# Optimization experiments

Measured on AMD Instinct MI355X. Metric: run time of the kernel, lower is better.

Reference implementation:

```python
import jax, jax.numpy as jnp
import numpy as np

DIM = 512
HEADS = 8
DIM_HEAD = 64
INNER = HEADS * DIM_HEAD  # 512
B, N = 4, 2048
EPS = 1e-5
DIFF = 1.0


def setup_inputs() -> dict:
    key = jax.random.key(0)
    ks = jax.random.split(key, 8)
    s = 1.0 / np.sqrt(DIM)
    return {
        "x": jax.random.normal(ks[0], (B, N, DIM), dtype=jnp.float32),
        "ln_w": jnp.ones((DIM,), jnp.float32),
        "ln_b": jnp.zeros((DIM,), jnp.float32),
        "wq": jax.random.uniform(ks[1], (INNER, DIM), jnp.float32, -s, s),
        "wk": jax.random.uniform(ks[2], (INNER, DIM), jnp.float32, -s, s),
        "wv_v": jax.random.uniform(ks[3], (INNER, DIM), jnp.float32, -s, s),  # weight-norm direction
        "wv_g": jax.random.uniform(ks[4], (INNER,), jnp.float32, 0.5, 1.5),   # weight-norm magnitude g
        "w_out": jax.random.uniform(ks[5], (DIM, INNER), jnp.float32, -s, s),
    }


def reference(x, ln_w, ln_b, wq, wk, wv_v, wv_g, w_out):
    # LayerNorm over last dim
    mu = jnp.mean(x, axis=-1, keepdims=True)
    var = jnp.mean(jnp.square(x - mu), axis=-1, keepdims=True)
    xn = (x - mu) * jax.lax.rsqrt(var + EPS) * ln_w + ln_b

    # weight-norm for V projection: W = g * v / ||v||_row (norm over dim=1)
    wv = wv_g[:, None] * wv_v / jnp.linalg.norm(wv_v, axis=1, keepdims=True)

    def proj(w):  # [b n (h d)] -> [b h n d]
        t = jnp.einsum('bnc,ec->bne', xn, w)
        return t.reshape(x.shape[0], x.shape[1], HEADS, DIM_HEAD).transpose(0, 2, 1, 3)

    q, k, v = proj(wq), proj(wk), proj(wv)

    scale = DIM_HEAD ** -0.5
    dots = jnp.einsum('bhid,bhjd->bhij', q, k) * scale
    attn = jax.nn.softmax(dots, axis=-1)
    out = jnp.einsum('bhij,bhjd->bhid', DIFF * attn, v)  # diff-scaled AV
    out = out.transpose(0, 2, 1, 3).reshape(x.shape[0], x.shape[1], INNER)
    return jnp.einsum('bne,ce->bnc', out, w_out)
```

## Files before the change

### kernel.cpp

```cpp
#include <hip/hip_runtime.h>
#include <hip/hip_bf16.h>
#include <stdint.h>

typedef __attribute__((ext_vector_type(8))) __bf16 bf16x8;
typedef __attribute__((ext_vector_type(8))) short short8;
typedef __attribute__((ext_vector_type(4))) float f32x4;

#define C1_QSCALE 0.18033688011112042f

__device__ __forceinline__ unsigned short f2bf(float f) {
    union { float f; unsigned int u; } v; v.f = f;
    unsigned int r = v.u + 0x7fffu + ((v.u >> 16) & 1u);
    return (unsigned short)(r >> 16);
}

__device__ __forceinline__ unsigned int cvtpk(float lo, float hi) {
    unsigned int r;
    asm("v_cvt_pk_bf16_f32 %0, %1, %2" : "=v"(r) : "v"(lo), "v"(hi));
    return r;
}

__device__ __forceinline__ float fexp2(float x) {
    float r;
    asm("v_exp_f32 %0, %1" : "=v"(r) : "v"(x));
    return r;
}

__device__ __forceinline__ void gl_lds16(const void* g, void* l) {
    __builtin_amdgcn_global_load_lds(
        (const __attribute__((address_space(1))) unsigned int*)g,
        (__attribute__((address_space(3))) unsigned int*)l, 16, 0, 0);
}

__device__ __forceinline__ f32x4 mfma16(bf16x8 a, bf16x8 b, f32x4 c) {
    return __builtin_amdgcn_mfma_f32_16x16x32_bf16(a, b, c, 0, 0, 0);
}

__global__ __launch_bounds__(256) void pre_kernel(
    const float* __restrict__ x, const float* __restrict__ lw,
    const float* __restrict__ lb, unsigned short* __restrict__ xn,
    const float* __restrict__ wq, const float* __restrict__ wk,
    const float* __restrict__ wv_v, const float* __restrict__ wv_g,
    const float* __restrict__ w_out,
    unsigned short* __restrict__ wqkv, unsigned short* __restrict__ woutb)
{
    const int t = threadIdx.x;
    if (blockIdx.x < 2048) {
        const int wv = t >> 6, l = t & 63;
        const int row = blockIdx.x * 4 + wv;
        const float* xr = x + (size_t)row * 512;
        const float4 a = *(const float4*)(xr + l*8);
        const float4 b = *(const float4*)(xr + l*8 + 4);
        float s  = (a.x + a.y) + (a.z + a.w) + (b.x + b.y) + (b.z + b.w);
        float sq = (a.x*a.x + a.y*a.y) + (a.z*a.z + a.w*a.w)
                 + (b.x*b.x + b.y*b.y) + (b.z*b.z + b.w*b.w);
        #pragma unroll
        for (int m = 1; m < 64; m <<= 1) { s += __shfl_xor(s, m); sq += __shfl_xor(sq, m); }
        const float mean = s * (1.f/512.f);
        const float var  = sq * (1.f/512.f) - mean*mean;
        const float rs   = rsqrtf(var + 1e-5f);
        const float4 w0 = *(const float4*)(lw + l*8);
        const float4 w1 = *(const float4*)(lw + l*8 + 4);
        const float4 c0 = *(const float4*)(lb + l*8);
        const float4 c1 = *(const float4*)(lb + l*8 + 4);
        uint4 o;
        o.x = cvtpk((a.x-mean)*rs*w0.x + c0.x, (a.y-mean)*rs*w0.y + c0.y);
        o.y = cvtpk((a.z-mean)*rs*w0.z + c0.z, (a.w-mean)*rs*w0.w + c0.w);
        o.z = cvtpk((b.x-mean)*rs*w1.x + c1.x, (b.y-mean)*rs*w1.y + c1.y);
        o.w = cvtpk((b.z-mean)*rs*w1.z + c1.z, (b.w-mean)*rs*w1.w + c1.w);
        *(uint4*)(xn + (size_t)row*512 + l*8) = o;
    } else {
        __shared__ float red[4];
        const int row = blockIdx.x - 2048;
        if (row < 1536) {
            const float* src;
            float scale = 1.0f;
            if (row < 512) src = wq + (size_t)row*512;
            else if (row < 1024) src = wk + (size_t)(row-512)*512;
            else {
                src = wv_v + (size_t)(row-1024)*512;
                float2 v = *(const float2*)(src + t*2);
                float sq = v.x*v.x + v.y*v.y;
                #pragma unroll
                for (int m = 1; m < 64; m <<= 1) sq += __shfl_xor(sq, m);
                if ((t & 63) == 0) red[t >> 6] = sq;
                __syncthreads();
                scale = wv_g[row-1024] * rsqrtf(red[0]+red[1]+red[2]+red[3]);
            }
            float2 v = *(const float2*)(src + t*2);
            ushort2 o; o.x = f2bf(v.x*scale); o.y = f2bf(v.y*scale);
            *(ushort2*)(wqkv + (size_t)row*512 + t*2) = o;
        } else {
            const int r = row - 1536;
            float2 v = *(const float2*)(w_out + (size_t)r*512 + t*2);
            ushort2 o; o.x = f2bf(v.x); o.y = f2bf(v.y);
            *(ushort2*)(woutb + (size_t)r*512 + t*2) = o;
        }
    }
}

template<int MODE, int BM, int BN>
__global__ __launch_bounds__(256) void gemm_nt(
    const unsigned short* __restrict__ A,
    const unsigned short* __restrict__ B,
    unsigned short* __restrict__ qo,
    unsigned short* __restrict__ ko,
    unsigned short* __restrict__ vo,
    float* __restrict__ outf)
{
    constexpr int MT  = BM / 32;
    constexpr int NT  = BN / 32;
    constexpr int ACH = BM / 64;
    constexpr int BCH = BN / 64;
    constexpr int BUFSZ = (BM + BN) * 64;
    __shared__ __align__(16) unsigned char L[3][BUFSZ];

    const int t = threadIdx.x;
    const int wv = t >> 6, l = t & 63;
    const int brow = blockIdx.x * BM;
    const int bcol = blockIdx.y * BN;
    const int wr = (wv >> 1) * (BM/2), wc = (wv & 1) * (BN/2);
    const int l15 = l & 15, l4 = l >> 4;
    const int rl  = l >> 2;
    const int cbl = l & 3;

    const f32x4 fz = {0.f, 0.f, 0.f, 0.f};
    f32x4 acc[MT][NT];
    #pragma unroll
    for (int i = 0; i < MT; ++i)
        #pragma unroll
        for (int j = 0; j < NT; ++j) acc[i][j] = fz;

    auto STAGE = [&](int ks, int buf) {
        #pragma unroll
        for (int i = 0; i < ACH; ++i) {
            const int c = wv*ACH + i;
            const int row = c*16 + rl;
            const int scb = cbl ^ ((row >> 1) & 3);
            gl_lds16(A + (size_t)(brow+row)*512 + ks*32 + scb*8, &L[buf][c*1024]);
        }
        #pragma unroll
        for (int i = 0; i < BCH; ++i) {
            const int c = wv*BCH + i;
            const int row = c*16 + rl;
            const int scb = cbl ^ ((row >> 1) & 3);
            gl_lds16(B + (size_t)(bcol+row)*512 + ks*32 + scb*8, &L[buf][BM*64 + c*1024]);
        }
    };

    STAGE(0, 0);
    STAGE(1, 1);

    int cur = 0;
    for (int ks = 0; ks < 16; ++ks) {
        if constexpr (ACH + BCH == 4) asm volatile("s_waitcnt vmcnt(4)" ::: "memory");
        else                          asm volatile("s_waitcnt vmcnt(3)" ::: "memory");
        __builtin_amdgcn_s_barrier();

        int nb = cur + 2; if (nb >= 3) nb -= 3;
        STAGE((ks + 2) & 15, nb);

        bf16x8 af[MT], bfr[NT];
        #pragma unroll
        for (int mt = 0; mt < MT; ++mt) {
            const int row = wr + mt*16 + l15;
            af[mt] = *(const bf16x8*)(&L[cur][0] + row*64 + ((l4 ^ ((row >> 1) & 3))*16));
        }
        #pragma unroll
        for (int nt = 0; nt < NT; ++nt) {
            const int row = wc + nt*16 + l15;
            bfr[nt] = *(const bf16x8*)(&L[cur][BM*64] + row*64 + ((l4 ^ ((row >> 1) & 3))*16));
        }
        __builtin_amdgcn_s_setprio(1);
        #pragma unroll
        for (int mt = 0; mt < MT; ++mt)
            #pragma unroll
            for (int nt = 0; nt < NT; ++nt)
                acc[mt][nt] = mfma16(af[mt], bfr[nt], acc[mt][nt]);
        __builtin_amdgcn_s_setprio(0);

        cur = (cur == 2) ? 0 : cur + 1;
    }

    if (MODE == 1) {
        #pragma unroll
        for (int mt = 0; mt < MT; ++mt)
            #pragma unroll
            for (int nt = 0; nt < NT; ++nt)
                #pragma unroll
                for (int r = 0; r < 4; ++r) {
                    const int grow = brow + wr + mt*16 + l4*4 + r;
                    const int gcol = bcol + wc + nt*16 + l15;
                    outf[(size_t)grow*512 + gcol] = acc[mt][nt][r];
                }
    } else if (bcol < 1024) {
        const bool isq = (bcol < 512);
        unsigned short* dst = isq ? qo : ko;
        const int csub = isq ? bcol : bcol - 512;
        const float scl = isq ? C1_QSCALE : 1.0f;
        #pragma unroll
        for (int mt = 0; mt < MT; ++mt)
            #pragma unroll
            for (int nt = 0; nt < NT; ++nt)
                #pragma unroll
                for (int r = 0; r < 4; ++r) {
                    const int grow = brow + wr + mt*16 + l4*4 + r;
                    const int gcol = csub + wc + nt*16 + l15;
                    const int h = gcol >> 6, d = gcol & 63;
                    const int bb = grow >> 11, n = grow & 2047;
                    dst[(((size_t)bb*8 + h)*2048 + n)*64 + d] = f2bf(acc[mt][nt][r]*scl);
                }
    } else {
        #pragma unroll
        for (int mt = 0; mt < MT; ++mt) {
            const int grow0 = brow + wr + mt*16 + l4*4;
            const int bb = grow0 >> 11;
            const int nb2 = (grow0 & 2047) & ~63;
            const int sigma0 = (mt>>1)*32 + l4*8 + (mt&1)*4;
            #pragma unroll
            for (int nt = 0; nt < NT; ++nt) {
                const int gcol = (bcol - 1024) + wc + nt*16 + l15;
                const int h = gcol >> 6, d = gcol & 63;
                uint2 ov;
                ov.x = cvtpk(acc[mt][nt][0], acc[mt][nt][1]);
                ov.y = cvtpk(acc[mt][nt][2], acc[mt][nt][3]);
                *(uint2*)(vo + ((size_t)(bb*8 + h)*64 + d)*2048 + nb2 + sigma0) = ov;
            }
        }
    }
}

__global__ __launch_bounds__(512, 4) void flash_attn(
    const unsigned short* __restrict__ Q,
    const unsigned short* __restrict__ K,
    const unsigned short* __restrict__ Vt,
    unsigned short* __restrict__ AO)
{
    __shared__ __align__(16) unsigned char Ks[3][8192];
    __shared__ __align__(16) unsigned char Vs[2][8192];
    const int t = threadIdx.x, wv = t >> 6, l = t & 63;
    const int l15 = l & 15, l4 = l >> 4;
    const int rl = l >> 3, cbl = l & 7;
    const int bh = blockIdx.x;
    const int q0 = blockIdx.y * 128;
    const size_t base = (size_t)bh * 2048 * 64;
    const int b = bh >> 3, h = bh & 7;

    bf16x8 qf[2];
    #pragma unroll
    for (int kk = 0; kk < 2; ++kk)
        qf[kk] = *(const bf16x8*)(Q + base + (size_t)(q0 + wv*16 + l15)*64 + kk*32 + 8*l4);

    const f32x4 fz = {0.f,0.f,0.f,0.f};
    f32x4 acco[4];
    float lrp = 0.f;
    #pragma unroll
    for (int dn = 0; dn < 4; ++dn) acco[dn] = fz;

    auto STAGE_K = [&](int kv, int buf) {
        const int row = wv*8 + rl;
        const int scb = cbl ^ (row & 7);
        gl_lds16(K + base + (size_t)(kv + row)*64 + scb*8, &Ks[buf][wv*1024]);
    };
    auto STAGE_V = [&](int kv, int buf) {
        const int row = wv*8 + rl;
        const int scb = cbl ^ (row & 7);
        gl_lds16(Vt + base + (size_t)row*2048 + kv + scb*8, &Vs[buf][wv*1024]);
    };

    STAGE_V(0, 0);
    STAGE_K(0, 0);
    STAGE_K(64, 1);

    int kb = 0, vb = 0;
    for (int it = 0; it < 32; ++it) {
        asm volatile("s_waitcnt vmcnt(1)" ::: "memory");
        __builtin_amdgcn_s_barrier();

        STAGE_V(((it + 1) & 31) * 64, vb ^ 1);
        STAGE_K(((it + 2) & 31) * 64, kb >= 1 ? kb - 1 : 2);

        bf16x8 kf[4][2];
        #pragma unroll
        for (int nt = 0; nt < 4; ++nt)
            #pragma unroll
            for (int kk = 0; kk < 2; ++kk) {
                const int row = nt*16 + l15;
                const int cb = kk*4 + l4;
                kf[nt][kk] = *(const bf16x8*)(&Ks[kb][0] + row*128 + ((cb ^ (row & 7))*16));
            }
        f32x4 st[4];
        __builtin_amdgcn_s_setprio(1);
        #pragma unroll
        for (int nt = 0; nt < 4; ++nt) {
            st[nt] = mfma16(kf[nt][0], qf[0], fz);
            st[nt] = mfma16(kf[nt][1], qf[1], st[nt]);
        }
        __builtin_amdgcn_s_setprio(0);

        float p[4][4];
        #pragma unroll
        for (int nt = 0; nt < 4; ++nt)
            #pragma unroll
            for (int r = 0; r < 4; ++r) p[nt][r] = fexp2(st[nt][r]);
        float s0 = (p[0][0]+p[0][1]) + (p[0][2]+p[0][3]);
        float s1 = (p[1][0]+p[1][1]) + (p[1][2]+p[1][3]);
        float s2 = (p[2][0]+p[2][1]) + (p[2][2]+p[2][3]);
        float s3 = (p[3][0]+p[3][1]) + (p[3][2]+p[3][3]);
        lrp += (s0 + s1) + (s2 + s3);

        bf16x8 pb[2];
        #pragma unroll
        for (int kh = 0; kh < 2; ++kh) {
            union { unsigned int u[4]; bf16x8 v; } pu;
            pu.u[0] = cvtpk(p[2*kh][0],   p[2*kh][1]);
            pu.u[1] = cvtpk(p[2*kh][2],   p[2*kh][3]);
            pu.u[2] = cvtpk(p[2*kh+1][0], p[2*kh+1][1]);
            pu.u[3] = cvtpk(p[2*kh+1][2], p[2*kh+1][3]);
            pb[kh] = pu.v;
        }

        __builtin_amdgcn_s_setprio(1);
        #pragma unroll
        for (int dn = 0; dn < 4; ++dn)
            #pragma unroll
            for (int kh = 0; kh < 2; ++kh) {
                const int row = dn*16 + l15;
                const int cb = kh*4 + l4;
                const bf16x8 vf = *(const bf16x8*)(&Vs[vb][0] + row*128 + ((cb ^ (row & 7))*16));
                acco[dn] = mfma16(vf, pb[kh], acco[dn]);
            }
        __builtin_amdgcn_s_setprio(0);

        kb = (kb == 2) ? 0 : kb + 1;
        vb ^= 1;
    }

    float lr = lrp;
    lr += __shfl_xor(lr, 16);
    lr += __shfl_xor(lr, 32);
    const float inv = 1.f / lr;
    const size_t nrow = (size_t)b*2048 + q0 + wv*16 + l15;
    #pragma unroll
    for (int dn = 0; dn < 4; ++dn) {
        uint2 ov;
        ov.x = cvtpk(acco[dn][0]*inv, acco[dn][1]*inv);
        ov.y = cvtpk(acco[dn][2]*inv, acco[dn][3]*inv);
        *(uint2*)(AO + nrow*512 + h*64 + dn*16 + l4*4) = ov;
    }
}

extern "C" void kernel_launch(void* const* d_in, const int* in_sizes, int n_in,
                              void* d_out, int out_size, void* d_ws, size_t ws_size,
                              hipStream_t stream)
{
    const float* x     = (const float*)d_in[0];
    const float* ln_w  = (const float*)d_in[1];
    const float* ln_b  = (const float*)d_in[2];
    const float* wq    = (const float*)d_in[3];
    const float* wk    = (const float*)d_in[4];
    const float* wv_v  = (const float*)d_in[5];
    const float* wv_g  = (const float*)d_in[6];
    const float* w_out = (const float*)d_in[7];
    float* out = (float*)d_out;
    char* ws = (char*)d_ws;

    unsigned short* xn    = (unsigned short*)(ws);
    unsigned short* ao    = (unsigned short*)(ws);
    unsigned short* wqkv  = (unsigned short*)(ws +  8388608);
    unsigned short* woutb = (unsigned short*)(ws +  9961472);
    unsigned short* q     = (unsigned short*)(ws + 10485760);
    unsigned short* k     = (unsigned short*)(ws + 18874368);
    unsigned short* vt    = (unsigned short*)(ws + 27262976);

    pre_kernel<<<dim3(4096), dim3(256), 0, stream>>>(x, ln_w, ln_b, xn,
        wq, wk, wv_v, wv_g, w_out, wqkv, woutb);
    gemm_nt<0,128,128><<<dim3(64, 12), dim3(256), 0, stream>>>(xn, wqkv, q, k, vt, (float*)nullptr);
    flash_attn<<<dim3(32, 16), dim3(512), 0, stream>>>(q, k, vt, ao);
    gemm_nt<1,128,64><<<dim3(64, 8), dim3(256), 0, stream>>>(ao, woutb,
        (unsigned short*)nullptr, (unsigned short*)nullptr, (unsigned short*)nullptr, out);
}
```

Baseline: 148.4 us.

## Process two query sub-tiles per wave to reuse K/V fragments in flash attention

Each wave now handles 32 query rows (two 16-row sub-tiles) instead of 16, so every K and V fragment read from LDS feeds two MFMAs. The block covers 256 queries, the grid along queries is halved, and launch bounds drop to 2 blocks per CU to allow more registers. The goal is to halve LDS traffic and global K/V staging per query. The cost is higher register pressure, fewer resident waves for hiding latency, and a smaller grid (256 blocks) that may leave some CUs idle.

```diff
diff --git a/kernel.cpp b/kernel.cpp
--- a/kernel.cpp
+++ b/kernel.cpp
@@ -230,7 +230,7 @@
     }
 }
 
-__global__ __launch_bounds__(512, 4) void flash_attn(
+__global__ __launch_bounds__(512, 2) void flash_attn(
     const unsigned short* __restrict__ Q,
     const unsigned short* __restrict__ K,
     const unsigned short* __restrict__ Vt,
@@ -242,20 +242,24 @@
     const int l15 = l & 15, l4 = l >> 4;
     const int rl = l >> 3, cbl = l & 7;
     const int bh = blockIdx.x;
-    const int q0 = blockIdx.y * 128;
+    const int q0 = blockIdx.y * 256;
     const size_t base = (size_t)bh * 2048 * 64;
     const int b = bh >> 3, h = bh & 7;
 
-    bf16x8 qf[2];
+    bf16x8 qf[2][2];
     #pragma unroll
-    for (int kk = 0; kk < 2; ++kk)
-        qf[kk] = *(const bf16x8*)(Q + base + (size_t)(q0 + wv*16 + l15)*64 + kk*32 + 8*l4);
+    for (int hq = 0; hq < 2; ++hq)
+        #pragma unroll
+        for (int kk = 0; kk < 2; ++kk)
+            qf[hq][kk] = *(const bf16x8*)(Q + base + (size_t)(q0 + wv*32 + hq*16 + l15)*64 + kk*32 + 8*l4);
 
     const f32x4 fz = {0.f,0.f,0.f,0.f};
-    f32x4 acco[4];
-    float lrp = 0.f;
+    f32x4 acco[2][4];
+    float lrp[2] = {0.f, 0.f};
     #pragma unroll
-    for (int dn = 0; dn < 4; ++dn) acco[dn] = fz;
+    for (int hq = 0; hq < 2; ++hq)
+        #pragma unroll
+        for (int dn = 0; dn < 4; ++dn) acco[hq][dn] = fz;
 
     auto STAGE_K = [&](int kv, int buf) {
         const int row = wv*8 + rl;
@@ -289,35 +293,39 @@
                 const int cb = kk*4 + l4;
                 kf[nt][kk] = *(const bf16x8*)(&Ks[kb][0] + row*128 + ((cb ^ (row & 7))*16));
             }
-        f32x4 st[4];
-        __builtin_amdgcn_s_setprio(1);
-        #pragma unroll
-        for (int nt = 0; nt < 4; ++nt) {
-            st[nt] = mfma16(kf[nt][0], qf[0], fz);
-            st[nt] = mfma16(kf[nt][1], qf[1], st[nt]);
-        }
-        __builtin_amdgcn_s_setprio(0);
-
-        float p[4][4];
-        #pragma unroll
-        for (int nt = 0; nt < 4; ++nt)
-            #pragma unroll
-            for (int r = 0; r < 4; ++r) p[nt][r] = fexp2(st[nt][r]);
-        float s0 = (p[0][0]+p[0][1]) + (p[0][2]+p[0][3]);
-        float s1 = (p[1][0]+p[1][1]) + (p[1][2]+p[1][3]);
-        float s2 = (p[2][0]+p[2][1]) + (p[2][2]+p[2][3]);
-        float s3 = (p[3][0]+p[3][1]) + (p[3][2]+p[3][3]);
-        lrp += (s0 + s1) + (s2 + s3);
-
-        bf16x8 pb[2];
-        #pragma unroll
-        for (int kh = 0; kh < 2; ++kh) {
-            union { unsigned int u[4]; bf16x8 v; } pu;
-            pu.u[0] = cvtpk(p[2*kh][0],   p[2*kh][1]);
-            pu.u[1] = cvtpk(p[2*kh][2],   p[2*kh][3]);
-            pu.u[2] = cvtpk(p[2*kh+1][0], p[2*kh+1][1]);
-            pu.u[3] = cvtpk(p[2*kh+1][2], p[2*kh+1][3]);
-            pb[kh] = pu.v;
+
+        bf16x8 pb[2][2];
+        #pragma unroll
+        for (int hq = 0; hq < 2; ++hq) {
+            f32x4 st[4];
+            __builtin_amdgcn_s_setprio(1);
+            #pragma unroll
+            for (int nt = 0; nt < 4; ++nt) {
+                st[nt] = mfma16(kf[nt][0], qf[hq][0], fz);
+                st[nt] = mfma16(kf[nt][1], qf[hq][1], st[nt]);
+            }
+            __builtin_amdgcn_s_setprio(0);
+
+            float p[4][4];
+            #pragma unroll
+            for (int nt = 0; nt < 4; ++nt)
+                #pragma unroll
+                for (int r = 0; r < 4; ++r) p[nt][r] = fexp2(st[nt][r]);
+            float s0 = (p[0][0]+p[0][1]) + (p[0][2]+p[0][3]);
+            float s1 = (p[1][0]+p[1][1]) + (p[1][2]+p[1][3]);
+            float s2 = (p[2][0]+p[2][1]) + (p[2][2]+p[2][3]);
+            float s3 = (p[3][0]+p[3][1]) + (p[3][2]+p[3][3]);
+            lrp[hq] += (s0 + s1) + (s2 + s3);
+
+            #pragma unroll
+            for (int kh = 0; kh < 2; ++kh) {
+                union { unsigned int u[4]; bf16x8 v; } pu;
+                pu.u[0] = cvtpk(p[2*kh][0],   p[2*kh][1]);
+                pu.u[1] = cvtpk(p[2*kh][2],   p[2*kh][3]);
+                pu.u[2] = cvtpk(p[2*kh+1][0], p[2*kh+1][1]);
+                pu.u[3] = cvtpk(p[2*kh+1][2], p[2*kh+1][3]);
+                pb[hq][kh] = pu.v;
+            }
         }
 
         __builtin_amdgcn_s_setprio(1);
@@ -328,7 +336,8 @@
                 const int row = dn*16 + l15;
                 const int cb = kh*4 + l4;
                 const bf16x8 vf = *(const bf16x8*)(&Vs[vb][0] + row*128 + ((cb ^ (row & 7))*16));
-                acco[dn] = mfma16(vf, pb[kh], acco[dn]);
+                acco[0][dn] = mfma16(vf, pb[0][kh], acco[0][dn]);
+                acco[1][dn] = mfma16(vf, pb[1][kh], acco[1][dn]);
             }
         __builtin_amdgcn_s_setprio(0);
 
@@ -336,17 +345,20 @@
         vb ^= 1;
     }
 
-    float lr = lrp;
-    lr += __shfl_xor(lr, 16);
-    lr += __shfl_xor(lr, 32);
-    const float inv = 1.f / lr;
-    const size_t nrow = (size_t)b*2048 + q0 + wv*16 + l15;
     #pragma unroll
-    for (int dn = 0; dn < 4; ++dn) {
-        uint2 ov;
-        ov.x = cvtpk(acco[dn][0]*inv, acco[dn][1]*inv);
-        ov.y = cvtpk(acco[dn][2]*inv, acco[dn][3]*inv);
-        *(uint2*)(AO + nrow*512 + h*64 + dn*16 + l4*4) = ov;
+    for (int hq = 0; hq < 2; ++hq) {
+        float lr = lrp[hq];
+        lr += __shfl_xor(lr, 16);
+        lr += __shfl_xor(lr, 32);
+        const float inv = 1.f / lr;
+        const size_t nrow = (size_t)b*2048 + q0 + wv*32 + hq*16 + l15;
+        #pragma unroll
+        for (int dn = 0; dn < 4; ++dn) {
+            uint2 ov;
+            ov.x = cvtpk(acco[hq][dn][0]*inv, acco[hq][dn][1]*inv);
+            ov.y = cvtpk(acco[hq][dn][2]*inv, acco[hq][dn][3]*inv);
+            *(uint2*)(AO + nrow*512 + h*64 + dn*16 + l4*4) = ov;
+        }
     }
 }
 
@@ -376,7 +388,7 @@
     pre_kernel<<<dim3(4096), dim3(256), 0, stream>>>(x, ln_w, ln_b, xn,
         wq, wk, wv_v, wv_g, w_out, wqkv, woutb);
     gemm_nt<0,128,128><<<dim3(64, 12), dim3(256), 0, stream>>>(xn, wqkv, q, k, vt, (float*)nullptr);
-    flash_attn<<<dim3(32, 16), dim3(512), 0, stream>>>(q, k, vt, ao);
+    flash_attn<<<dim3(32, 8), dim3(512), 0, stream>>>(q, k, vt, ao);
     gemm_nt<1,128,64><<<dim3(64, 8), dim3(256), 0, stream>>>(ao, woutb,
         (unsigned short*)nullptr, (unsigned short*)nullptr, (unsigned short*)nullptr, out);
 }
```

After: 158.8 us. 7.0% more time.
